# Kernel optimization log

Measured on AMD Instinct MI355X. Metric: run time of the kernel, lower is better.

Reference implementation:

```python
import jax, jax.numpy as jnp
import numpy as np

N_SP = 32  # number of superpixels, hardcoded in the original module


def setup_inputs() -> dict:
    key = jax.random.key(0)
    k1, k2 = jax.random.split(key)
    b, c, h, w = 16, 64, 512, 512
    features = jax.random.normal(k1, (b, c, h, w), dtype=jnp.float32)
    superpixel_indices = jax.random.randint(k2, (b, h, w), 0, N_SP, dtype=jnp.int32)
    return {"features": features, "superpixel_indices": superpixel_indices}


def reference(features, superpixel_indices):
    b, c, h, w = features.shape
    # [b, h*w, c]
    feats = jnp.transpose(features, (0, 2, 3, 1)).reshape(b * h * w, c)
    # offset segment ids so all batches reduce in one segment_sum pass
    ids = (superpixel_indices.reshape(b, h * w)
           + (jnp.arange(b, dtype=superpixel_indices.dtype)[:, None] * N_SP)).reshape(-1)
    sums = jax.ops.segment_sum(feats, ids, num_segments=b * N_SP)          # [b*N, c]
    counts = jax.ops.segment_sum(jnp.ones((b * h * w,), feats.dtype), ids,
                                 num_segments=b * N_SP)                     # [b*N]
    # mean per superpixel; empty superpixels stay zero (matches torch init)
    sp = jnp.where(counts[:, None] > 0,
                   sums / jnp.maximum(counts[:, None], 1.0),
                   0.0).reshape(b, N_SP, c)
    # pairwise: sim[i,j] = 1 - 0.5 * ||sp_i - sp_j||^2  (N=32, tiny)
    diff = sp[:, :, None, :] - sp[:, None, :, :]        # [b, N, N, c]
    sim = 1.0 - 0.5 * jnp.sum(diff * diff, axis=-1)     # [b, N, N]
    return sp, sim
```

## Files before the change

kernel.cpp:

```cpp
#include <hip/hip_runtime.h>

#define NSP 32
#define BB  16
#define CC  64
#define HW  (512 * 512)

#define BLOCK  256
#define CHUNK  8192
#define NCHUNK (HW / CHUNK)
#define KIT    (CHUNK / 4 / BLOCK)
#define STR    (NSP + 1)

#define BAR() asm volatile("s_waitcnt lgkmcnt(0)\n\ts_barrier" ::: "memory")

__global__ __launch_bounds__(BLOCK) void sp_accum(const float* __restrict__ feats,
                                                  const int*   __restrict__ spidx,
                                                  float*       __restrict__ sums  ,
                                                  float*       __restrict__ counts)
{
    __shared__ float2 s_priv[BLOCK][STR];
    __shared__ float2 s_pe[8][NSP];
    __shared__ float2 s_po[8][NSP];

    const int tid  = threadIdx.x;
    const int b    = blockIdx.y;
    const int pix0 = blockIdx.x * CHUNK;
    const int bin  = tid & 31;
    const int grp  = tid >> 5;

    float2* row = s_priv[tid];

    uchar4 uu[KIT];
    {
        const int4* ip = (const int4*)(spidx + (size_t)b * HW + pix0);
#pragma unroll
        for (int k = 0; k < KIT; ++k) {
            int4 v = ip[k * BLOCK + tid];
            uu[k] = make_uchar4((unsigned char)(v.x & 31), (unsigned char)(v.y & 31),
                                (unsigned char)(v.z & 31), (unsigned char)(v.w & 31));
        }
    }
#pragma unroll
    for (int s = 0; s < STR; ++s) row[s] = make_float2(0.f, 0.f);

    const float* fb = feats + (size_t)b * CC * HW + pix0;
    float4 pre[KIT][2];
#pragma unroll
    for (int k = 0; k < KIT; ++k) {
        pre[k][0] = ((const float4*)fb)[k * BLOCK + tid];
        pre[k][1] = ((const float4*)(fb + (size_t)HW))[k * BLOCK + tid];
    }

#pragma unroll
    for (int k = 0; k < KIT; ++k) {
        row[uu[k].x].x += 1.f;
        row[uu[k].y].x += 1.f;
        row[uu[k].z].x += 1.f;
        row[uu[k].w].x += 1.f;
    }
    BAR();
    {
        float a = 0.f;
#pragma unroll
        for (int m = 0; m < BLOCK / 8; ++m) a += s_priv[grp + m * 8][bin].x;
        s_pe[grp][bin].x = a;
    }
    BAR();
#pragma unroll
    for (int s = 0; s < STR; ++s) row[s] = make_float2(0.f, 0.f);
    if (tid < NSP) {
        float r = 0.f;
#pragma unroll
        for (int g = 0; g < 8; ++g) r += s_pe[g][tid].x;
        atomicAdd(&counts[b * NSP + tid], r);
    }

    for (int p = 0; p < CC / 2; ++p) {
        const int ch0 = 2 * p;
        float2 (*part)[NSP] = (p & 1) ? s_po : s_pe;

#pragma unroll
        for (int k = 0; k < KIT; ++k) {
            const uchar4 u = uu[k];
            const float4 a = pre[k][0], c = pre[k][1];
            float2 t0 = row[u.x], t1 = row[u.y], t2 = row[u.z], t3 = row[u.w];
            float2 cx = make_float2(a.x, c.x);
            float2 cy = make_float2(a.y, c.y);
            float2 cz = make_float2(a.z, c.z);
            float2 cw = make_float2(a.w, c.w);
            const bool ky  = (u.y == u.x);
            const bool kz1 = (u.z == u.x), kz2 = (u.z == u.y);
            const bool kw1 = (u.w == u.x), kw2 = (u.w == u.y), kw3 = (u.w == u.z);
            if (ky)  { cx.x += cy.x; cx.y += cy.y; }
            if (kz1) { cx.x += cz.x; cx.y += cz.y; }
            else if (kz2) { cy.x += cz.x; cy.y += cz.y; }
            if (kw1) { cx.x += cw.x; cx.y += cw.y; }
            else if (kw2) { cy.x += cw.x; cy.y += cw.y; }
            else if (kw3) { cz.x += cw.x; cz.y += cw.y; }
            const unsigned wy = ky ? 32u : (unsigned)u.y;
            const unsigned wz = (kz1 | kz2) ? 32u : (unsigned)u.z;
            const unsigned ww = (kw1 | kw2 | kw3) ? 32u : (unsigned)u.w;
            row[u.x] = make_float2(t0.x + cx.x, t0.y + cx.y);
            row[wy]  = make_float2(t1.x + cy.x, t1.y + cy.y);
            row[wz]  = make_float2(t2.x + cz.x, t2.y + cz.y);
            row[ww]  = make_float2(t3.x + cw.x, t3.y + cw.y);
        }
        if (p + 1 < CC / 2) {
            const float* g0 = fb + (size_t)(ch0 + 2) * HW;
#pragma unroll
            for (int k = 0; k < KIT; ++k) {
                pre[k][0] = ((const float4*)g0)[k * BLOCK + tid];
                pre[k][1] = ((const float4*)(g0 + (size_t)HW))[k * BLOCK + tid];
            }
        }
        BAR();
        {
            float2 acc = make_float2(0.f, 0.f);
#pragma unroll
            for (int m = 0; m < BLOCK / 8; ++m) {
                float2 v = s_priv[grp + m * 8][bin];
                acc.x += v.x; acc.y += v.y;
            }
            part[grp][bin] = acc;
        }
        BAR();
#pragma unroll
        for (int s = 0; s < STR; ++s) row[s] = make_float2(0.f, 0.f);
        if (tid < NSP) {
            float2 r = part[0][tid];
#pragma unroll
            for (int g = 1; g < 8; ++g) { r.x += part[g][tid].x; r.y += part[g][tid].y; }
            atomicAdd(&sums[((size_t)b * CC + ch0)     * NSP + tid], r.x);
            atomicAdd(&sums[((size_t)b * CC + ch0 + 1) * NSP + tid], r.y);
        }
    }
}

__global__ __launch_bounds__(BLOCK) void sp_finalize(const float* __restrict__ sums,
                                                     const float* __restrict__ counts,
                                                     float*       __restrict__ out)
{
    __shared__ float s_sp[NSP][CC + 1];
    const int b   = blockIdx.x;
    const int tid = threadIdx.x;

    for (int i = tid; i < NSP * CC; i += BLOCK) {
        int sp = i >> 6, c = i & 63;
        float cnt = counts[b * NSP + sp];
        float s   = sums[((size_t)b * CC + c) * NSP + sp];
        float v   = (cnt > 0.0f) ? (s / cnt) : 0.0f;
        s_sp[sp][c] = v;
        out[(size_t)b * NSP * CC + (size_t)sp * CC + c] = v;
    }
    __syncthreads();

    for (int p = tid; p < NSP * NSP; p += BLOCK) {
        int i = p >> 5, j = p & 31;
        float acc = 0.0f;
#pragma unroll
        for (int c = 0; c < CC; ++c) {
            float d = s_sp[i][c] - s_sp[j][c];
            acc = fmaf(d, d, acc);
        }
        out[(size_t)BB * NSP * CC + (size_t)b * NSP * NSP + p] = 1.0f - 0.5f * acc;
    }
}

extern "C" void kernel_launch(void* const* d_in, const int* in_sizes, int n_in,
                              void* d_out, int out_size, void* d_ws, size_t ws_size,
                              hipStream_t stream)
{
    const float* feats = (const float*)d_in[0];
    const int*   spidx = (const int*)d_in[1];
    float*       out   = (float*)d_out;

    float* sums   = (float*)d_ws;
    float* counts = sums + (size_t)BB * CC * NSP;

    hipMemsetAsync(d_ws, 0, ((size_t)BB * CC * NSP + (size_t)BB * NSP) * sizeof(float), stream);

    dim3 g1(NCHUNK, BB);
    sp_accum<<<g1, BLOCK, 0, stream>>>(feats, spidx, sums, counts);

    sp_finalize<<<BB, BLOCK, 0, stream>>>(sums, counts, out);
}
```

Before: 214.4 us.

## Double-buffer feature prefetch two channel-pairs ahead and simplify LDS bin updates

Splits the per-thread register prefetch into two buffers, so global loads for channels four ahead are issued while the current pair is accumulated. The goal is more outstanding memory traffic and more hidden load latency in this bandwidth-heavy scatter kernel. It also replaces the duplicate-index merging logic with plain sequential read-modify-write on the private LDS row. That cuts ALU and compare work but serialises the LDS updates into dependent chains. The second buffer roughly doubles the prefetch register footprint.

```diff
diff --git a/kernel.cpp b/kernel.cpp
--- a/kernel.cpp
+++ b/kernel.cpp
@@ -44,11 +44,16 @@
     for (int s = 0; s < STR; ++s) row[s] = make_float2(0.f, 0.f);
 
     const float* fb = feats + (size_t)b * CC * HW + pix0;
-    float4 pre[KIT][2];
+    float4 preA[KIT][2], preB[KIT][2];
 #pragma unroll
     for (int k = 0; k < KIT; ++k) {
-        pre[k][0] = ((const float4*)fb)[k * BLOCK + tid];
-        pre[k][1] = ((const float4*)(fb + (size_t)HW))[k * BLOCK + tid];
+        preA[k][0] = ((const float4*)(fb))[k * BLOCK + tid];
+        preA[k][1] = ((const float4*)(fb + (size_t)HW))[k * BLOCK + tid];
+    }
+#pragma unroll
+    for (int k = 0; k < KIT; ++k) {
+        preB[k][0] = ((const float4*)(fb + (size_t)2 * HW))[k * BLOCK + tid];
+        preB[k][1] = ((const float4*)(fb + (size_t)3 * HW))[k * BLOCK + tid];
     }
 
 #pragma unroll
@@ -75,38 +80,19 @@
         atomicAdd(&counts[b * NSP + tid], r);
     }
 
-    for (int p = 0; p < CC / 2; ++p) {
-        const int ch0 = 2 * p;
-        float2 (*part)[NSP] = (p & 1) ? s_po : s_pe;
-
+    auto pass = [&](float4 (&pre)[KIT][2], int ch0, float2 (*part)[NSP]) {
 #pragma unroll
         for (int k = 0; k < KIT; ++k) {
             const uchar4 u = uu[k];
             const float4 a = pre[k][0], c = pre[k][1];
-            float2 t0 = row[u.x], t1 = row[u.y], t2 = row[u.z], t3 = row[u.w];
-            float2 cx = make_float2(a.x, c.x);
-            float2 cy = make_float2(a.y, c.y);
-            float2 cz = make_float2(a.z, c.z);
-            float2 cw = make_float2(a.w, c.w);
-            const bool ky  = (u.y == u.x);
-            const bool kz1 = (u.z == u.x), kz2 = (u.z == u.y);
-            const bool kw1 = (u.w == u.x), kw2 = (u.w == u.y), kw3 = (u.w == u.z);
-            if (ky)  { cx.x += cy.x; cx.y += cy.y; }
-            if (kz1) { cx.x += cz.x; cx.y += cz.y; }
-            else if (kz2) { cy.x += cz.x; cy.y += cz.y; }
-            if (kw1) { cx.x += cw.x; cx.y += cw.y; }
-            else if (kw2) { cy.x += cw.x; cy.y += cw.y; }
-            else if (kw3) { cz.x += cw.x; cz.y += cw.y; }
-            const unsigned wy = ky ? 32u : (unsigned)u.y;
-            const unsigned wz = (kz1 | kz2) ? 32u : (unsigned)u.z;
-            const unsigned ww = (kw1 | kw2 | kw3) ? 32u : (unsigned)u.w;
-            row[u.x] = make_float2(t0.x + cx.x, t0.y + cx.y);
-            row[wy]  = make_float2(t1.x + cy.x, t1.y + cy.y);
-            row[wz]  = make_float2(t2.x + cz.x, t2.y + cz.y);
-            row[ww]  = make_float2(t3.x + cw.x, t3.y + cw.y);
+            float2 t;
+            t = row[u.x]; t.x += a.x; t.y += c.x; row[u.x] = t;
+            t = row[u.y]; t.x += a.y; t.y += c.y; row[u.y] = t;
+            t = row[u.z]; t.x += a.z; t.y += c.z; row[u.z] = t;
+            t = row[u.w]; t.x += a.w; t.y += c.w; row[u.w] = t;
         }
-        if (p + 1 < CC / 2) {
-            const float* g0 = fb + (size_t)(ch0 + 2) * HW;
+        if (ch0 + 4 < CC) {
+            const float* g0 = fb + (size_t)(ch0 + 4) * HW;
 #pragma unroll
             for (int k = 0; k < KIT; ++k) {
                 pre[k][0] = ((const float4*)g0)[k * BLOCK + tid];
@@ -133,6 +119,11 @@
             atomicAdd(&sums[((size_t)b * CC + ch0)     * NSP + tid], r.x);
             atomicAdd(&sums[((size_t)b * CC + ch0 + 1) * NSP + tid], r.y);
         }
+    };
+
+    for (int p = 0; p < CC / 2; p += 2) {
+        pass(preA, 2 * p,     s_pe);
+        pass(preB, 2 * p + 2, s_po);
     }
 }
 
```

New measurement: 219.5 us. +2.4%, slower.
